# Kernel optimization log

Hardware: AMD Instinct MI355X
Metric: run time of the kernel (lower is better)

Reference implementation:

```python
import jax, jax.numpy as jnp
import numpy as np


def setup_inputs() -> dict:
    key = jax.random.key(0)
    k1, k2, k3 = jax.random.split(key, 3)
    B, S, IN, OUT = 2, 4096, 4096, 11008
    # int8 activations and weights, matching torch.randint(-127, 127, ...)
    x = jax.random.randint(k1, (B, S, IN), -127, 127, dtype=jnp.int8)
    weight = jax.random.randint(k2, (OUT, IN), -127, 127, dtype=jnp.int8)
    bias = jax.random.normal(k3, (1, OUT), dtype=jnp.float32)
    alpha = jnp.array(1e-3, dtype=jnp.float32)  # input_scale * weight_scale
    return {"x": x, "weight": weight, "bias": bias, "alpha": alpha}


def reference(x, weight, bias, alpha):
    # y = SiLU(alpha * (x_i8 @ W_i8^T) + beta * bias), beta = 1.0, output fp32
    x_shape = x.shape
    x2d = x.reshape(-1, x_shape[-1])  # [N, in]
    acc = jnp.matmul(x2d.astype(jnp.int32), weight.T.astype(jnp.int32))  # [N, out] int32
    y = alpha * acc.astype(jnp.float32) + bias  # fused dequant + bias epilogue
    y = y * jax.nn.sigmoid(y)  # SiLU
    return y.reshape(*x_shape[:-1], -1)
```

## Files before the change

### kernel.cpp

```cpp
#include <hip/hip_runtime.h>
#include <stdint.h>

#define TM 128
#define TN 128
#define BK 128

typedef __attribute__((ext_vector_type(4)))  int i32x4;
typedef __attribute__((ext_vector_type(16))) int i32x16;

__device__ __forceinline__ void async16(const void* g, void* l) {
    __builtin_amdgcn_global_load_lds(
        (const __attribute__((address_space(1))) unsigned int*)g,
        (__attribute__((address_space(3))) unsigned int*)l,
        16 , 0 , 0 );
}

__global__ void pack_both(const int4* __restrict__ sx, int* __restrict__ dx, int nx4,
                          const int4* __restrict__ sw, int* __restrict__ dw, int nw4) {
    int idx    = blockIdx.x * blockDim.x + threadIdx.x;
    int stride = gridDim.x * blockDim.x;
    for (int i = idx; i < nx4; i += stride) {
        int4 a = sx[i];
        dx[i] = (a.x & 0xFF) | ((a.y & 0xFF) << 8) | ((a.z & 0xFF) << 16) | (a.w << 24);
    }
    for (int i = idx; i < nw4; i += stride) {
        int4 a = sw[i];
        dw[i] = (a.x & 0xFF) | ((a.y & 0xFF) << 8) | ((a.z & 0xFF) << 16) | (a.w << 24);
    }
}

__global__ __launch_bounds__(256, 2) void w8a8_silu_kernel(
    const int8_t* __restrict__ x, const int8_t* __restrict__ w,
    const float* __restrict__ bias, const float* __restrict__ alpha_p,
    float* __restrict__ out, int M, int N, int K, int nbn)
{
    __shared__ int8_t lds_a[TM * BK];
    __shared__ int8_t lds_b[TN * BK];

    const int tid  = threadIdx.x;
    const int lane = tid & 63;
    const int wave = tid >> 6;

    int bid = blockIdx.x;
    const int nwg = gridDim.x;
    if ((nwg & 7) == 0) bid = (bid & 7) * (nwg >> 3) + (bid >> 3);
    const int bm = bid / nbn;
    const int bn = bid - bm * nbn;

    const int srow  = tid >> 3;
    const int skoff = (((tid & 7) ^ (srow & 7)) << 4);
    const int8_t* gA = x + ((size_t)bm * TM + srow) * K + skoff;
    const int8_t* gB = w + ((size_t)bn * TN + srow) * K + skoff;
    int8_t* lA = lds_a + tid * 16;
    int8_t* lB = lds_b + tid * 16;

    const int wr  = (wave >> 1) * 64;
    const int wc  = (wave & 1) * 64;
    const int l31 = lane & 31;
    const int q2  = lane >> 5;
    const int xl  = lane & 7;

    i32x16 acc[2][2] = {};

    for (int k0 = 0; k0 < K; k0 += BK) {
        __syncthreads();
#pragma unroll
        for (int j = 0; j < 4; ++j) {
            async16(gA + (size_t)(j * 32) * K + k0, lA + j * 4096);
            async16(gB + (size_t)(j * 32) * K + k0, lB + j * 4096);
        }
        __syncthreads();

#pragma unroll
        for (int ks = 0; ks < 4; ++ks) {
            i32x4 af[2], bf[2];
            const int ck = ((ks * 2 + q2) ^ xl) << 4;
#pragma unroll
            for (int t = 0; t < 2; ++t) {
                af[t] = *(const i32x4*)(lds_a + ((wr + t * 32 + l31) << 7) + ck);
                bf[t] = *(const i32x4*)(lds_b + ((wc + t * 32 + l31) << 7) + ck);
            }
            acc[0][0] = __builtin_amdgcn_mfma_i32_32x32x32_i8(af[0], bf[0], acc[0][0], 0, 0, 0);
            acc[0][1] = __builtin_amdgcn_mfma_i32_32x32x32_i8(af[0], bf[1], acc[0][1], 0, 0, 0);
            acc[1][0] = __builtin_amdgcn_mfma_i32_32x32x32_i8(af[1], bf[0], acc[1][0], 0, 0, 0);
            acc[1][1] = __builtin_amdgcn_mfma_i32_32x32x32_i8(af[1], bf[1], acc[1][1], 0, 0, 0);
        }
    }

    const float alpha = *alpha_p;
    const int rowb = bm * TM + wr;
    const int colb = bn * TN + wc;
#pragma unroll
    for (int ct = 0; ct < 2; ++ct) {
        const int col = colb + ct * 32 + l31;
        const float bv = bias[col];
#pragma unroll
        for (int rt = 0; rt < 2; ++rt) {
#pragma unroll
            for (int r = 0; r < 16; ++r) {
                const int row = rowb + rt * 32 + (r & 3) + ((r >> 2) << 3) + (q2 << 2);
                float y = fmaf(alpha, (float)acc[rt][ct][r], bv);
                out[(size_t)row * N + col] = y / (1.0f + __expf(-y));
            }
        }
    }
}

extern "C" void kernel_launch(void* const* d_in, const int* in_sizes, int n_in,
                              void* d_out, int out_size, void* d_ws, size_t ws_size,
                              hipStream_t stream) {
    const int*   x32   = (const int*)d_in[0];
    const int*   w32   = (const int*)d_in[1];
    const float* bias  = (const float*)d_in[2];
    const float* alpha = (const float*)d_in[3];
    float*       out   = (float*)d_out;

    const int N = in_sizes[2];
    const int K = in_sizes[1] / N;
    const int M = in_sizes[0] / K;

    int8_t* x8 = (int8_t*)d_ws;
    int8_t* w8 = x8 + (size_t)M * K;

    const int nx4 = (int)(((size_t)M * K) / 4);
    const int nw4 = (int)(((size_t)N * K) / 4);
    pack_both<<<2048, 256, 0, stream>>>((const int4*)x32, (int*)x8, nx4,
                                        (const int4*)w32, (int*)w8, nw4);

    const int nbm = M / TM, nbn = N / TN;
    w8a8_silu_kernel<<<nbm * nbn, 256, 0, stream>>>(x8, w8, bias, alpha, out, M, N, K, nbn);
}
```

Baseline: 982.7 us.

## Double-buffer LDS tiles with BK=64 to overlap global loads with MFMA

Halves the K tile to 64 and allocates two LDS buffers per operand, prefetching the next tile via global_load_lds before computing the current one. A single barrier per iteration replaces the two barriers that serialized load and compute. The swizzle is changed to a rotation scheme suited to 64-byte rows. Shorter tiles mean more loop iterations and barrier overhead per K.

```diff
diff --git a/kernel.cpp b/kernel.cpp
--- a/kernel.cpp
+++ b/kernel.cpp
@@ -3,7 +3,7 @@
 
 #define TM 128
 #define TN 128
-#define BK 128
+#define BK 64
 
 typedef __attribute__((ext_vector_type(4)))  int i32x4;
 typedef __attribute__((ext_vector_type(16))) int i32x16;
@@ -34,8 +34,8 @@
     const float* __restrict__ bias, const float* __restrict__ alpha_p,
     float* __restrict__ out, int M, int N, int K, int nbn)
 {
-    __shared__ int8_t lds_a[TM * BK];
-    __shared__ int8_t lds_b[TN * BK];
+    __shared__ int8_t lds_a[2][TM * BK];
+    __shared__ int8_t lds_b[2][TN * BK];
 
     const int tid  = threadIdx.x;
     const int lane = tid & 63;
@@ -47,44 +47,55 @@
     const int bm = bid / nbn;
     const int bn = bid - bm * nbn;
 
-    const int srow  = tid >> 3;
-    const int skoff = (((tid & 7) ^ (srow & 7)) << 4);
+    const int srow  = tid >> 2;
+    const int skoff = ((((tid & 3) - ((tid >> 3) & 3)) & 3) << 4);
     const int8_t* gA = x + ((size_t)bm * TM + srow) * K + skoff;
     const int8_t* gB = w + ((size_t)bn * TN + srow) * K + skoff;
-    int8_t* lA = lds_a + tid * 16;
-    int8_t* lB = lds_b + tid * 16;
+    const int ldst = tid * 16;
 
     const int wr  = (wave >> 1) * 64;
     const int wc  = (wave & 1) * 64;
     const int l31 = lane & 31;
     const int q2  = lane >> 5;
-    const int xl  = lane & 7;
+    const int cq  = (l31 >> 1) & 3;
 
     i32x16 acc[2][2] = {};
 
-    for (int k0 = 0; k0 < K; k0 += BK) {
-        __syncthreads();
+    const int NT = K / BK;
+
+    async16(gA,                  &lds_a[0][ldst]);
+    async16(gA + (size_t)64 * K, &lds_a[0][4096 + ldst]);
+    async16(gB,                  &lds_b[0][ldst]);
+    async16(gB + (size_t)64 * K, &lds_b[0][4096 + ldst]);
+    __syncthreads();
+
+    int cur = 0;
+    for (int t = 0; t < NT; ++t) {
+        if (t + 1 < NT) {
+            const size_t kn = (size_t)(t + 1) * BK;
+            int8_t* la = lds_a[cur ^ 1];
+            int8_t* lb = lds_b[cur ^ 1];
+            async16(gA + kn,                  la + ldst);
+            async16(gA + (size_t)64 * K + kn, la + 4096 + ldst);
+            async16(gB + kn,                  lb + ldst);
+            async16(gB + (size_t)64 * K + kn, lb + 4096 + ldst);
+        }
+        const int8_t* la = lds_a[cur];
+        const int8_t* lb = lds_b[cur];
 #pragma unroll
-        for (int j = 0; j < 4; ++j) {
-            async16(gA + (size_t)(j * 32) * K + k0, lA + j * 4096);
-            async16(gB + (size_t)(j * 32) * K + k0, lB + j * 4096);
+        for (int ks = 0; ks < 2; ++ks) {
+            const int ck = (((ks * 2 + q2) + cq) & 3) << 4;
+            i32x4 a0 = *(const i32x4*)(la + ((wr +      l31) << 6) + ck);
+            i32x4 a1 = *(const i32x4*)(la + ((wr + 32 + l31) << 6) + ck);
+            i32x4 b0 = *(const i32x4*)(lb + ((wc +      l31) << 6) + ck);
+            i32x4 b1 = *(const i32x4*)(lb + ((wc + 32 + l31) << 6) + ck);
+            acc[0][0] = __builtin_amdgcn_mfma_i32_32x32x32_i8(a0, b0, acc[0][0], 0, 0, 0);
+            acc[0][1] = __builtin_amdgcn_mfma_i32_32x32x32_i8(a0, b1, acc[0][1], 0, 0, 0);
+            acc[1][0] = __builtin_amdgcn_mfma_i32_32x32x32_i8(a1, b0, acc[1][0], 0, 0, 0);
+            acc[1][1] = __builtin_amdgcn_mfma_i32_32x32x32_i8(a1, b1, acc[1][1], 0, 0, 0);
         }
         __syncthreads();
-
-#pragma unroll
-        for (int ks = 0; ks < 4; ++ks) {
-            i32x4 af[2], bf[2];
-            const int ck = ((ks * 2 + q2) ^ xl) << 4;
-#pragma unroll
-            for (int t = 0; t < 2; ++t) {
-                af[t] = *(const i32x4*)(lds_a + ((wr + t * 32 + l31) << 7) + ck);
-                bf[t] = *(const i32x4*)(lds_b + ((wc + t * 32 + l31) << 7) + ck);
-            }
-            acc[0][0] = __builtin_amdgcn_mfma_i32_32x32x32_i8(af[0], bf[0], acc[0][0], 0, 0, 0);
-            acc[0][1] = __builtin_amdgcn_mfma_i32_32x32x32_i8(af[0], bf[1], acc[0][1], 0, 0, 0);
-            acc[1][0] = __builtin_amdgcn_mfma_i32_32x32x32_i8(af[1], bf[0], acc[1][0], 0, 0, 0);
-            acc[1][1] = __builtin_amdgcn_mfma_i32_32x32x32_i8(af[1], bf[1], acc[1][1], 0, 0, 0);
-        }
+        cur ^= 1;
     }
 
     const float alpha = *alpha_p;
```

After: 1.005 ms. +2.3%, slower.
